# Kernel tuning notes

Measured on AMD Instinct MI355X. Metric: run time of the kernel, lower is better.

Reference implementation:

```python
import jax, jax.numpy as jnp
import numpy as np

NUM_EMBEDDINGS = 4096  # lexicon_size
EMBEDDING_DIM = 256    # feature_size
BETA = 0.25
N_CODES = 32768        # flattened batch of encoder outputs


def setup_inputs() -> dict:
    key = jax.random.key(0)
    k1, k2 = jax.random.split(key)
    inputs = jax.random.normal(k1, (N_CODES, EMBEDDING_DIM), dtype=jnp.float32)
    # nn.Embedding init: uniform(-1/K, 1/K)
    embed_w = jax.random.uniform(
        k2, (NUM_EMBEDDINGS, EMBEDDING_DIM), dtype=jnp.float32,
        minval=-1.0 / NUM_EMBEDDINGS, maxval=1.0 / NUM_EMBEDDINGS)
    return {"inputs": inputs, "embed_w": embed_w}


def reference(inputs, embed_w):
    # Faithful translation of VectorQuantizer_gcn.forward (index=None path).
    flat = inputs.reshape(-1, EMBEDDING_DIM)               # [N, D]
    distances = (jnp.sum(flat * flat, axis=1, keepdims=True)
                 + jnp.sum(embed_w * embed_w, axis=1)
                 - 2.0 * jnp.einsum('nd,kd->nk', flat, embed_w))
    encoding_indices = jnp.argmin(distances, axis=1)        # [N]
    # one-hot scatter + matmul in torch == gather of codebook rows
    quantized = jnp.take(embed_w, encoding_indices, axis=0)  # [N, D]
    sg = jax.lax.stop_gradient
    commitloss = (jnp.mean((sg(quantized) - flat) ** 2)
                  + BETA * jnp.mean((quantized - sg(flat)) ** 2))
    # straight-through estimator
    quantized_st = flat + sg(quantized - flat)
    contrastloss = jnp.float32(0.0)
    return (quantized_st, encoding_indices[:, None], commitloss, contrastloss)
```

## Files before the change

kernel.cpp:

```cpp
#include <hip/hip_runtime.h>
#include <cstdint>
#include <cstddef>

#define D_DIM 256
#define NT 64
#define SROWS 256
#define SNS 4
#define MARGIN 1.3e-3f
#define RCAP 2048

typedef unsigned int u32;
typedef unsigned short u16;
typedef unsigned long long u64;
typedef __attribute__((ext_vector_type(8))) short s16x8;
typedef __attribute__((ext_vector_type(4))) float f32x4;

static __device__ __forceinline__ u16 f2bf(float f) {
  u32 u = __float_as_uint(f);
  return (u16)((u + 0x7FFFu + ((u >> 16) & 1u)) >> 16);
}

static __device__ __forceinline__ float np_pw128_sq(const float* __restrict__ p) {
  float r0, r1, r2, r3, r4, r5, r6, r7;
  {
    const float4 a = *reinterpret_cast<const float4*>(p);
    const float4 b = *reinterpret_cast<const float4*>(p + 4);
    r0 = __fmul_rn(a.x, a.x); r1 = __fmul_rn(a.y, a.y);
    r2 = __fmul_rn(a.z, a.z); r3 = __fmul_rn(a.w, a.w);
    r4 = __fmul_rn(b.x, b.x); r5 = __fmul_rn(b.y, b.y);
    r6 = __fmul_rn(b.z, b.z); r7 = __fmul_rn(b.w, b.w);
  }
  #pragma unroll
  for (int i = 8; i < 128; i += 8) {
    const float4 a = *reinterpret_cast<const float4*>(p + i);
    const float4 b = *reinterpret_cast<const float4*>(p + i + 4);
    r0 = __fadd_rn(r0, __fmul_rn(a.x, a.x));
    r1 = __fadd_rn(r1, __fmul_rn(a.y, a.y));
    r2 = __fadd_rn(r2, __fmul_rn(a.z, a.z));
    r3 = __fadd_rn(r3, __fmul_rn(a.w, a.w));
    r4 = __fadd_rn(r4, __fmul_rn(b.x, b.x));
    r5 = __fadd_rn(r5, __fmul_rn(b.y, b.y));
    r6 = __fadd_rn(r6, __fmul_rn(b.z, b.z));
    r7 = __fadd_rn(r7, __fmul_rn(b.w, b.w));
  }
  const float s01 = __fadd_rn(r0, r1);
  const float s23 = __fadd_rn(r2, r3);
  const float s45 = __fadd_rn(r4, r5);
  const float s67 = __fadd_rn(r6, r7);
  return __fadd_rn(__fadd_rn(s01, s23), __fadd_rn(s45, s67));
}

static __device__ __forceinline__ float exact_dot256(
    const float* __restrict__ xp, const float* __restrict__ wp) {
  float a = 0.f;
  #pragma unroll 8
  for (int d4 = 0; d4 < 64; ++d4) {
    const float4 xv = *reinterpret_cast<const float4*>(xp + d4 * 4);
    const float4 wv = *reinterpret_cast<const float4*>(wp + d4 * 4);
    a = fmaf(xv.x, wv.x, a);
    a = fmaf(xv.y, wv.y, a);
    a = fmaf(xv.z, wv.z, a);
    a = fmaf(xv.w, wv.w, a);
  }
  return a;
}

__global__ __launch_bounds__(256) void cvt_kernel(
    const float* __restrict__ X, const float* __restrict__ W,
    u16* __restrict__ Xb, u16* __restrict__ Wb, int nx4, int nw4) {
  const int tid = blockIdx.x * blockDim.x + threadIdx.x;
  const int stride = gridDim.x * blockDim.x;
  for (int g = tid; g < nx4; g += stride) {
    const float4 v = reinterpret_cast<const float4*>(X)[g];
    ushort4 o; o.x = f2bf(v.x); o.y = f2bf(v.y); o.z = f2bf(v.z); o.w = f2bf(v.w);
    reinterpret_cast<ushort4*>(Xb)[g] = o;
  }
  for (int g = tid; g < nw4; g += stride) {
    const float4 v = reinterpret_cast<const float4*>(W)[g];
    ushort4 o; o.x = f2bf(v.x); o.y = f2bf(v.y); o.z = f2bf(v.z); o.w = f2bf(v.w);
    reinterpret_cast<ushort4*>(Wb)[g] = o;
  }
}

#define DPP_RED_STEP(CTRL)                                                     \
  {                                                                            \
    const float ov = __uint_as_float((u32)__builtin_amdgcn_update_dpp(         \
        0, (int)__float_as_uint(v), CTRL, 0xF, 0xF, true));                    \
    const int oi = __builtin_amdgcn_update_dpp(0, idx, CTRL, 0xF, 0xF, true);  \
    if (ov > v || (ov == v && oi < idx)) { v = ov; idx = oi; }                 \
  }

__global__ __launch_bounds__(256, 2) void vq_sweep(
    const u16* __restrict__ Xb, const u16* __restrict__ Wb,
    float* __restrict__ tm, u16* __restrict__ ti, int K) {
  __shared__ u16 Ws[NT * D_DIM];

  const int t = threadIdx.x;
  const int wv = t >> 6;
  const int lane = t & 63;
  const int l15 = lane & 15, lhi = lane >> 4;
  const int rb = blockIdx.x >> 2;
  const int hs = blockIdx.x & 3;
  const int row0 = rb * SROWS;
  const int wrow0 = row0 + wv * 64;
  const int c00 = hs * (K / SNS);

  s16x8 af[4][8];
  #pragma unroll
  for (int rt = 0; rt < 4; ++rt)
    #pragma unroll
    for (int kc = 0; kc < 8; ++kc)
      af[rt][kc] = *reinterpret_cast<const s16x8*>(
          Xb + (size_t)(wrow0 + rt * 16 + l15) * D_DIM + kc * 32 + lhi * 8);

  const int NTILES = K / SNS / NT;
  for (int ct = 0; ct < NTILES; ++ct) {
    __syncthreads();
    {
      const int code = t >> 2, k4 = t & 3;
      const u16* wp = Wb + (size_t)(c00 + ct * NT + code) * D_DIM;
      #pragma unroll
      for (int kk = 0; kk < 8; ++kk) {
        const int kc8 = kk * 4 + k4;
        *reinterpret_cast<uint4*>(&Ws[(kc8 * NT + code) * 8]) =
            *reinterpret_cast<const uint4*>(wp + kc8 * 8);
      }
    }
    __syncthreads();

    f32x4 acc[4][4];
    #pragma unroll
    for (int rt = 0; rt < 4; ++rt)
      #pragma unroll
      for (int c = 0; c < 4; ++c) acc[rt][c] = f32x4{0.f, 0.f, 0.f, 0.f};

    #pragma unroll
    for (int kc = 0; kc < 8; ++kc) {
      s16x8 bf[4];
      #pragma unroll
      for (int c = 0; c < 4; ++c)
        bf[c] = *reinterpret_cast<const s16x8*>(
            &Ws[((kc * 4 + lhi) * NT + c * 16 + l15) * 8]);
      #pragma unroll
      for (int c = 0; c < 4; ++c) {
        acc[0][c] = __builtin_amdgcn_mfma_f32_16x16x32_bf16(af[0][kc], bf[c], acc[0][c], 0, 0, 0);
        acc[1][c] = __builtin_amdgcn_mfma_f32_16x16x32_bf16(af[1][kc], bf[c], acc[1][c], 0, 0, 0);
        acc[2][c] = __builtin_amdgcn_mfma_f32_16x16x32_bf16(af[2][kc], bf[c], acc[2][c], 0, 0, 0);
        acc[3][c] = __builtin_amdgcn_mfma_f32_16x16x32_bf16(af[3][kc], bf[c], acc[3][c], 0, 0, 0);
      }
    }

    #pragma unroll
    for (int rt = 0; rt < 4; ++rt)
      #pragma unroll
      for (int r = 0; r < 4; ++r) {
        float v = acc[rt][0][r];
        int idx = c00 + ct * NT + l15;
        #pragma unroll
        for (int c = 1; c < 4; ++c) {
          const float vc = acc[rt][c][r];
          const int ic = c00 + ct * NT + c * 16 + l15;
          if (vc > v) { v = vc; idx = ic; }
        }
        DPP_RED_STEP(0x121)
        DPP_RED_STEP(0x122)
        DPP_RED_STEP(0x124)
        DPP_RED_STEP(0x128)
        if (l15 == 0) {
          const int row = wrow0 + rt * 16 + lhi * 4 + r;
          const int tile = hs * NTILES + ct;
          tm[(size_t)row * 64 + tile] = v;
          ti[(size_t)row * 64 + tile] = (u16)idx;
        }
      }
  }
}

__global__ __launch_bounds__(256) void vq_resolve(
    const float* __restrict__ X, const float* __restrict__ W,
    const float* __restrict__ tm, const u16* __restrict__ ti,
    float* __restrict__ outI, int K) {
  __shared__ float ftmp[256];
  __shared__ float xsqs[128];
  __shared__ u64 best64[128];
  __shared__ uint2 list[RCAP];
  __shared__ int cnt;

  const int t = threadIdx.x;
  const int row0 = blockIdx.x * 128;

  {
    const int r = t >> 1, half = t & 1;
    ftmp[t] = np_pw128_sq(X + (size_t)(row0 + r) * D_DIM + half * 128);
  }
  if (t == 0) cnt = 0;
  __syncthreads();
  if (t < 128) {
    xsqs[t] = __fadd_rn(ftmp[2 * t], ftmp[2 * t + 1]);
    best64[t] = 0xFFFFFFFFFFFFFFFFull;
  }
  __syncthreads();

  if (t < 128) {
    const int row = row0 + t;
    const float4* tm4 = reinterpret_cast<const float4*>(tm + (size_t)row * 64);
    float4 q[16];
    float rowmax = -3.4e38f;
    #pragma unroll
    for (int i = 0; i < 16; ++i) {
      q[i] = tm4[i];
      rowmax = fmaxf(rowmax, fmaxf(fmaxf(q[i].x, q[i].y), fmaxf(q[i].z, q[i].w)));
    }
    const float thr = rowmax - MARGIN;
    const u16* tir = ti + (size_t)row * 64;
    #pragma unroll
    for (int i = 0; i < 16; ++i) {
      #pragma unroll
      for (int j = 0; j < 4; ++j) {
        const float v = (j == 0) ? q[i].x : (j == 1) ? q[i].y
                      : (j == 2) ? q[i].z : q[i].w;
        if (v >= thr) {
          const int code = (int)tir[i * 4 + j] & (K - 1);
          const int idx = atomicAdd(&cnt, 1);
          if (idx < RCAP) {
            uint2 e; e.x = (u32)t; e.y = (u32)code;
            list[idx] = e;
          } else {
            const float a = exact_dot256(X + (size_t)row * D_DIM,
                                         W + (size_t)code * D_DIM);
            const float dist = __fsub_rn(xsqs[t], 2.0f * a);
            const u64 packed = ((u64)__float_as_uint(dist) << 32) | (u32)code;
            atomicMin(&best64[t], packed);
          }
        }
      }
    }
  }
  __syncthreads();

  int n = cnt; if (n > RCAP) n = RCAP;
  for (int i = t; i < n; i += 256) {
    const uint2 e = list[i];
    const float a = exact_dot256(X + (size_t)(row0 + (int)e.x) * D_DIM,
                                 W + (size_t)e.y * D_DIM);
    const float dist = __fsub_rn(xsqs[e.x], 2.0f * a);
    const u64 packed = ((u64)__float_as_uint(dist) << 32) | e.y;
    atomicMin(&best64[e.x], packed);
  }
  __syncthreads();

  if (t < 128) outI[row0 + t] = (float)(u32)(best64[t] & 0xFFFFFFFFull);
}

__global__ __launch_bounds__(256) void vq_gather(
    const float* __restrict__ X, const float* __restrict__ W,
    const float* __restrict__ outI, float* __restrict__ outQ,
    double* __restrict__ partials, int K) {
  __shared__ double dsum[256];
  const int t = threadIdx.x;
  const int r = t >> 1, half = t & 1;
  const int row = blockIdx.x * 128 + r;
  const int ix = (int)outI[row];

  double csum = 0.0;
  {
    const int k = ix & (K - 1);
    const float* xp = X + (size_t)row * D_DIM + half * 128;
    const float* wp = W + (size_t)k * D_DIM + half * 128;
    float* op = outQ + (size_t)row * D_DIM + half * 128;
    #pragma unroll 4
    for (int i = 0; i < 128; i += 4) {
      const float4 xv = *reinterpret_cast<const float4*>(xp + i);
      const float4 wv = *reinterpret_cast<const float4*>(wp + i);
      const float d0 = __fsub_rn(wv.x, xv.x), d1 = __fsub_rn(wv.y, xv.y);
      const float d2 = __fsub_rn(wv.z, xv.z), d3 = __fsub_rn(wv.w, xv.w);
      csum += (double)d0 * d0 + (double)d1 * d1 + (double)d2 * d2 + (double)d3 * d3;
      float4 o;
      o.x = __fadd_rn(xv.x, d0);
      o.y = __fadd_rn(xv.y, d1);
      o.z = __fadd_rn(xv.z, d2);
      o.w = __fadd_rn(xv.w, d3);
      *reinterpret_cast<float4*>(op + i) = o;
    }
  }
  dsum[t] = csum;
  __syncthreads();
  for (int s = 128; s > 0; s >>= 1) {
    if (t < s) dsum[t] += dsum[t + s];
    __syncthreads();
  }
  if (t == 0) partials[blockIdx.x] = dsum[0];
}

__global__ __launch_bounds__(256) void vq_finalize(
    const double* __restrict__ partials, float* __restrict__ outS,
    double invCount) {
  __shared__ double dsum[256];
  const int t = threadIdx.x;
  dsum[t] = partials[t];
  __syncthreads();
  for (int s = 128; s > 0; s >>= 1) {
    if (t < s) dsum[t] += dsum[t + s];
    __syncthreads();
  }
  if (t == 0) {
    const float m = (float)(dsum[0] * invCount);
    outS[0] = __fadd_rn(m, __fmul_rn(0.25f, m));
    outS[1] = 0.f;
  }
}

__global__ void zero_out_kernel(float* __restrict__ out, int n) {
  const int i = blockIdx.x * blockDim.x + threadIdx.x;
  const int stride = gridDim.x * blockDim.x;
  for (int j = i; j < n; j += stride) out[j] = 0.f;
}
__global__ void beacon_kernel(float* __restrict__ out, float v) {
  if (threadIdx.x == 0) out[0] = v;
}

extern "C" void kernel_launch(void* const* d_in, const int* in_sizes, int n_in,
                              void* d_out, int out_size, void* d_ws, size_t ws_size,
                              hipStream_t stream) {
  float* outF = (float*)d_out;

  float hostBeacon = 0.f;
  if (n_in != 2) hostBeacon = 21.f;
  else if (in_sizes[0] != 32768 * 256) hostBeacon = 23.f;
  else if (in_sizes[1] != 4096 * 256) hostBeacon = 25.f;
  else if (ws_size < 4096) hostBeacon = 27.f;
  else if (out_size != 32768 * 256 + 32768 + 2) hostBeacon = 29.f;

  if (hostBeacon != 0.f) {
    zero_out_kernel<<<dim3(2048), dim3(256), 0, stream>>>(outF, out_size);
    beacon_kernel<<<dim3(1), dim3(64), 0, stream>>>(outF, hostBeacon);
    return;
  }

  const float* X = (const float*)d_in[0];
  const float* W = (const float*)d_in[1];
  const int N = 32768, K = 4096;

  double* partials = (double*)d_ws;
  float* outQ = outF;
  float* outI = outQ + (size_t)N * D_DIM;
  float* outS = outI + N;

  u16* Xb = (u16*)outQ;
  u16* Wb = (u16*)((char*)d_out + 16777216);
  float* tmv = (float*)((char*)d_out + 18874368);
  u16* tiv = (u16*)((char*)d_out + 27262976);

  cvt_kernel<<<dim3(2048), dim3(256), 0, stream>>>(
      X, W, Xb, Wb, N * D_DIM / 4, K * D_DIM / 4);
  vq_sweep<<<dim3((N / SROWS) * SNS), dim3(256), 0, stream>>>(Xb, Wb, tmv, tiv, K);
  vq_resolve<<<dim3(N / 128), dim3(256), 0, stream>>>(X, W, tmv, tiv, outI, K);
  vq_gather<<<dim3(N / 128), dim3(256), 0, stream>>>(X, W, outI, outQ, partials, K);
  vq_finalize<<<dim3(1), dim3(256), 0, stream>>>(partials, outS,
                                                 1.0 / ((double)N * D_DIM));
}
```

Baseline: 244.5 us.

## Fuse X bf16 conversion into sweep, read W fragments directly, stage tile results in LDS

The fp32 inputs are now converted to bf16 inside the sweep kernel, so the X pass in the convert kernel and the bf16 copy of X in the output buffer are gone. Codebook fragments are loaded straight from global/L2 with no LDS staging and no per-tile barriers. Rows per block drop from 256 to 128 and occupancy rises to 3 blocks per CU. Per-tile argmax results are collected in shared memory and written out as coalesced vectors at the end. In exchange, every wave re-reads the W fragments from cache with less reuse per block, which raises L2 traffic.

```diff
diff --git a/kernel.cpp b/kernel.cpp
--- a/kernel.cpp
+++ b/kernel.cpp
@@ -4,7 +4,7 @@
 
 #define D_DIM 256
 #define NT 64
-#define SROWS 256
+#define SROWS 128
 #define SNS 4
 #define MARGIN 1.3e-3f
 #define RCAP 2048
@@ -65,16 +65,10 @@
   return a;
 }
 
-__global__ __launch_bounds__(256) void cvt_kernel(
-    const float* __restrict__ X, const float* __restrict__ W,
-    u16* __restrict__ Xb, u16* __restrict__ Wb, int nx4, int nw4) {
+__global__ __launch_bounds__(256) void cvtW_kernel(
+    const float* __restrict__ W, u16* __restrict__ Wb, int nw4) {
   const int tid = blockIdx.x * blockDim.x + threadIdx.x;
   const int stride = gridDim.x * blockDim.x;
-  for (int g = tid; g < nx4; g += stride) {
-    const float4 v = reinterpret_cast<const float4*>(X)[g];
-    ushort4 o; o.x = f2bf(v.x); o.y = f2bf(v.y); o.z = f2bf(v.z); o.w = f2bf(v.w);
-    reinterpret_cast<ushort4*>(Xb)[g] = o;
-  }
   for (int g = tid; g < nw4; g += stride) {
     const float4 v = reinterpret_cast<const float4*>(W)[g];
     ushort4 o; o.x = f2bf(v.x); o.y = f2bf(v.y); o.z = f2bf(v.z); o.w = f2bf(v.w);
@@ -90,10 +84,11 @@
     if (ov > v || (ov == v && oi < idx)) { v = ov; idx = oi; }                 \
   }
 
-__global__ __launch_bounds__(256, 2) void vq_sweep(
-    const u16* __restrict__ Xb, const u16* __restrict__ Wb,
+__global__ __launch_bounds__(256, 3) void vq_sweep(
+    const float* __restrict__ X, const u16* __restrict__ Wb,
     float* __restrict__ tm, u16* __restrict__ ti, int K) {
-  __shared__ u16 Ws[NT * D_DIM];
+  __shared__ float tmS[SROWS][16];
+  __shared__ u16 tiS[SROWS][16];
 
   const int t = threadIdx.x;
   const int wv = t >> 6;
@@ -102,35 +97,32 @@
   const int rb = blockIdx.x >> 2;
   const int hs = blockIdx.x & 3;
   const int row0 = rb * SROWS;
-  const int wrow0 = row0 + wv * 64;
+  const int wrow0 = row0 + wv * 32;
   const int c00 = hs * (K / SNS);
 
-  s16x8 af[4][8];
+  s16x8 af[2][8];
   #pragma unroll
-  for (int rt = 0; rt < 4; ++rt)
-    #pragma unroll
-    for (int kc = 0; kc < 8; ++kc)
-      af[rt][kc] = *reinterpret_cast<const s16x8*>(
-          Xb + (size_t)(wrow0 + rt * 16 + l15) * D_DIM + kc * 32 + lhi * 8);
+  for (int rt = 0; rt < 2; ++rt)
+    #pragma unroll
+    for (int kc = 0; kc < 8; ++kc) {
+      const float* xp = X + (size_t)(wrow0 + rt * 16 + l15) * D_DIM + kc * 32 + lhi * 8;
+      const float4 a = *reinterpret_cast<const float4*>(xp);
+      const float4 b = *reinterpret_cast<const float4*>(xp + 4);
+      s16x8 v;
+      v[0] = (short)f2bf(a.x); v[1] = (short)f2bf(a.y);
+      v[2] = (short)f2bf(a.z); v[3] = (short)f2bf(a.w);
+      v[4] = (short)f2bf(b.x); v[5] = (short)f2bf(b.y);
+      v[6] = (short)f2bf(b.z); v[7] = (short)f2bf(b.w);
+      af[rt][kc] = v;
+    }
 
   const int NTILES = K / SNS / NT;
   for (int ct = 0; ct < NTILES; ++ct) {
-    __syncthreads();
-    {
-      const int code = t >> 2, k4 = t & 3;
-      const u16* wp = Wb + (size_t)(c00 + ct * NT + code) * D_DIM;
-      #pragma unroll
-      for (int kk = 0; kk < 8; ++kk) {
-        const int kc8 = kk * 4 + k4;
-        *reinterpret_cast<uint4*>(&Ws[(kc8 * NT + code) * 8]) =
-            *reinterpret_cast<const uint4*>(wp + kc8 * 8);
-      }
-    }
-    __syncthreads();
-
-    f32x4 acc[4][4];
-    #pragma unroll
-    for (int rt = 0; rt < 4; ++rt)
+    const int cb = c00 + ct * NT;
+
+    f32x4 acc[2][4];
+    #pragma unroll
+    for (int rt = 0; rt < 2; ++rt)
       #pragma unroll
       for (int c = 0; c < 4; ++c) acc[rt][c] = f32x4{0.f, 0.f, 0.f, 0.f};
 
@@ -140,26 +132,24 @@
       #pragma unroll
       for (int c = 0; c < 4; ++c)
         bf[c] = *reinterpret_cast<const s16x8*>(
-            &Ws[((kc * 4 + lhi) * NT + c * 16 + l15) * 8]);
+            Wb + (size_t)(cb + c * 16 + l15) * D_DIM + kc * 32 + lhi * 8);
       #pragma unroll
       for (int c = 0; c < 4; ++c) {
         acc[0][c] = __builtin_amdgcn_mfma_f32_16x16x32_bf16(af[0][kc], bf[c], acc[0][c], 0, 0, 0);
         acc[1][c] = __builtin_amdgcn_mfma_f32_16x16x32_bf16(af[1][kc], bf[c], acc[1][c], 0, 0, 0);
-        acc[2][c] = __builtin_amdgcn_mfma_f32_16x16x32_bf16(af[2][kc], bf[c], acc[2][c], 0, 0, 0);
-        acc[3][c] = __builtin_amdgcn_mfma_f32_16x16x32_bf16(af[3][kc], bf[c], acc[3][c], 0, 0, 0);
       }
     }
 
     #pragma unroll
-    for (int rt = 0; rt < 4; ++rt)
+    for (int rt = 0; rt < 2; ++rt)
       #pragma unroll
       for (int r = 0; r < 4; ++r) {
         float v = acc[rt][0][r];
-        int idx = c00 + ct * NT + l15;
+        int idx = cb + l15;
         #pragma unroll
         for (int c = 1; c < 4; ++c) {
           const float vc = acc[rt][c][r];
-          const int ic = c00 + ct * NT + c * 16 + l15;
+          const int ic = cb + c * 16 + l15;
           if (vc > v) { v = vc; idx = ic; }
         }
         DPP_RED_STEP(0x121)
@@ -167,12 +157,28 @@
         DPP_RED_STEP(0x124)
         DPP_RED_STEP(0x128)
         if (l15 == 0) {
-          const int row = wrow0 + rt * 16 + lhi * 4 + r;
-          const int tile = hs * NTILES + ct;
-          tm[(size_t)row * 64 + tile] = v;
-          ti[(size_t)row * 64 + tile] = (u16)idx;
+          const int lr = wv * 32 + rt * 16 + lhi * 4 + r;
+          tmS[lr][ct] = v;
+          tiS[lr][ct] = (u16)idx;
         }
       }
+  }
+  __syncthreads();
+
+  {
+    const int r = t >> 1, half = t & 1;
+    const int row = row0 + r;
+    *reinterpret_cast<float4*>(&tm[(size_t)row * 64 + hs * 16 + half * 8]) =
+        *reinterpret_cast<const float4*>(&tmS[r][half * 8]);
+    *reinterpret_cast<float4*>(&tm[(size_t)row * 64 + hs * 16 + half * 8 + 4]) =
+        *reinterpret_cast<const float4*>(&tmS[r][half * 8 + 4]);
+  }
+  if (t < SROWS) {
+    const int row = row0 + t;
+    *reinterpret_cast<uint4*>(&ti[(size_t)row * 64 + hs * 16]) =
+        *reinterpret_cast<const uint4*>(&tiS[t][0]);
+    *reinterpret_cast<uint4*>(&ti[(size_t)row * 64 + hs * 16 + 8]) =
+        *reinterpret_cast<const uint4*>(&tiS[t][8]);
   }
 }
 
@@ -346,14 +352,12 @@
   float* outI = outQ + (size_t)N * D_DIM;
   float* outS = outI + N;
 
-  u16* Xb = (u16*)outQ;
   u16* Wb = (u16*)((char*)d_out + 16777216);
   float* tmv = (float*)((char*)d_out + 18874368);
   u16* tiv = (u16*)((char*)d_out + 27262976);
 
-  cvt_kernel<<<dim3(2048), dim3(256), 0, stream>>>(
-      X, W, Xb, Wb, N * D_DIM / 4, K * D_DIM / 4);
-  vq_sweep<<<dim3((N / SROWS) * SNS), dim3(256), 0, stream>>>(Xb, Wb, tmv, tiv, K);
+  cvtW_kernel<<<dim3(512), dim3(256), 0, stream>>>(W, Wb, K * D_DIM / 4);
+  vq_sweep<<<dim3((N / SROWS) * SNS), dim3(256), 0, stream>>>(X, Wb, tmv, tiv, K);
   vq_resolve<<<dim3(N / 128), dim3(256), 0, stream>>>(X, W, tmv, tiv, outI, K);
   vq_gather<<<dim3(N / 128), dim3(256), 0, stream>>>(X, W, outI, outQ, partials, K);
   vq_finalize<<<dim3(1), dim3(256), 0, stream>>>(partials, outS,
```

New measurement: 438.9 us. 1.8x slower.
